# Kernel optimization log

Hardware: AMD Instinct MI355X
Metric: run time of the kernel (lower is better)

The kernel has to match this reference:

```python
import jax, jax.numpy as jnp
import numpy as np

H = 8      # num heads
D = 16     # head dim
HID = 128  # hidden_channels = H*D
L = 2      # num layers
NT = [30000, 15000, 2000]  # compound, protein, herb
# edge types as (src_type_idx, dst_type_idx); node types: 0=compound,1=protein,2=herb
ETYPES = [(2, 0), (0, 2), (0, 1), (1, 0), (1, 1)]


def segment_softmax(a, seg, n):
    m = jax.ops.segment_max(a, seg, num_segments=n)
    e = jnp.exp(a - m[seg])
    s = jax.ops.segment_sum(e, seg, num_segments=n)
    return e / (s[seg] + 1e-16)


def hgt_layer(xs, edges, Wk, bk, Wq, bq, Wv, bv, Wa, ba, skip, a_rel, m_rel, p_rel):
    ns = [x.shape[0] for x in xs]
    k = [(xs[t] @ Wk[t] + bk[t]).reshape(ns[t], H, D) for t in range(3)]
    q = [(xs[t] @ Wq[t] + bq[t]).reshape(ns[t], H, D) for t in range(3)]
    v = [(xs[t] @ Wv[t] + bv[t]).reshape(ns[t], H, D) for t in range(3)]
    out = [jnp.zeros((ns[t], H, D), xs[t].dtype) for t in range(3)]
    scale = 1.0 / np.sqrt(D).astype(np.float32)
    for e, (st, dt) in enumerate(ETYPES):
        src, dst = edges[e]
        # relation-specific key/value transforms per head, then gather per edge
        ke = jnp.einsum('nhd,hde->nhe', k[st], a_rel[e])[src]   # [E,H,D]
        ve = jnp.einsum('nhd,hde->nhe', v[st], m_rel[e])[src]   # [E,H,D]
        qe = q[dt][dst]                                          # [E,H,D]
        alpha = (qe * ke).sum(-1) * p_rel[e] * scale             # [E,H]
        alpha = segment_softmax(alpha, dst, ns[dt])
        out[dt] = out[dt] + jax.ops.segment_sum(alpha[..., None] * ve, dst, num_segments=ns[dt])
    res = []
    for t in range(3):
        o = jax.nn.gelu(out[t].reshape(ns[t], H * D)) @ Wa[t] + ba[t]
        beta = jax.nn.sigmoid(skip[t])
        res.append(beta * o + (1.0 - beta) * xs[t])
    return res


def setup_inputs() -> dict:
    key = jax.random.key(0)
    ks = jax.random.split(key, 40)
    i = 0
    def nk():
        nonlocal i
        i += 1
        return ks[i - 1]
    inp = {}
    inp['x_compound'] = jax.random.normal(nk(), (NT[0], 512), jnp.float32)
    inp['x_protein'] = jax.random.normal(nk(), (NT[1], 1024), jnp.float32)
    inp['x_herb'] = jax.random.normal(nk(), (NT[2], 128), jnp.float32)
    E = [100000, 100000, 200000, 200000, 150000]
    for e, (st, dt) in enumerate(ETYPES):
        inp[f'e{e}_src'] = jax.random.randint(nk(), (E[e],), 0, NT[st], jnp.int32)
        inp[f'e{e}_dst'] = jax.random.randint(nk(), (E[e],), 0, NT[dt], jnp.int32)
    def lin(k, fi, fo):
        return jax.random.normal(k, (fi, fo), jnp.float32) / np.sqrt(fi).astype(np.float32)
    inp['Wc'] = lin(nk(), 512, HID); inp['bc'] = jnp.zeros((HID,), jnp.float32)
    inp['Wp'] = lin(nk(), 1024, HID); inp['bp'] = jnp.zeros((HID,), jnp.float32)
    inp['Wh'] = lin(nk(), 128, HID); inp['bh'] = jnp.zeros((HID,), jnp.float32)
    for nm in ['Wk', 'Wq', 'Wv', 'Wa']:
        inp[nm] = jax.random.normal(nk(), (L, 3, HID, HID), jnp.float32) / np.sqrt(HID).astype(np.float32)
    for nm in ['bk', 'bq', 'bv', 'ba']:
        inp[nm] = jnp.zeros((L, 3, HID), jnp.float32)
    inp['skip'] = jnp.ones((L, 3), jnp.float32)
    inp['a_rel'] = jax.random.normal(nk(), (L, 5, H, D, D), jnp.float32) / np.sqrt(D).astype(np.float32)
    inp['m_rel'] = jax.random.normal(nk(), (L, 5, H, D, D), jnp.float32) / np.sqrt(D).astype(np.float32)
    inp['p_rel'] = jnp.ones((L, 5, H), jnp.float32)
    return inp


def reference(x_compound, x_protein, x_herb,
              e0_src, e0_dst, e1_src, e1_dst, e2_src, e2_dst, e3_src, e3_dst, e4_src, e4_dst,
              Wc, bc, Wp, bp, Wh, bh, Wk, bk, Wq, bq, Wv, bv, Wa, ba, skip, a_rel, m_rel, p_rel):
    xs = [x_compound @ Wc + bc, x_protein @ Wp + bp, x_herb @ Wh + bh]
    edges = [(e0_src, e0_dst), (e1_src, e1_dst), (e2_src, e2_dst), (e3_src, e3_dst), (e4_src, e4_dst)]
    for l in range(L):
        xs = hgt_layer(xs, edges, Wk[l], bk[l], Wq[l], bq[l], Wv[l], bv[l], Wa[l], ba[l],
                       skip[l], a_rel[l], m_rel[l], p_rel[l])
    # concatenate [compound; protein; herb] node embeddings along node axis
    return jnp.concatenate(xs, axis=0)
```

## Files before the change

### kernel.cpp

```cpp
#include <hip/hip_runtime.h>
#include <math.h>

#define HID 128

typedef __bf16 bf16x8 __attribute__((ext_vector_type(8)));
typedef float f32x4 __attribute__((ext_vector_type(4)));

__device__ __forceinline__ float gelu_f(float x) {
    float x3 = x*x*x;
    return 0.5f*x*(1.f + tanhf(0.7978845608028654f*(x + 0.044715f*x3)));
}
__device__ __forceinline__ unsigned short bf16_rn(float x) {
    unsigned int u = __float_as_uint(x);
    unsigned int r = (u + 0x7FFFu + ((u >> 16) & 1u)) >> 16;
    return (unsigned short)r;
}
__device__ __forceinline__ void split2(float x, unsigned short& h, unsigned short& l) {
    h = bf16_rn(x);
    float hf = __uint_as_float(((unsigned int)h) << 16);
    l = bf16_rn(x - hf);
}
__device__ __forceinline__ float blo(unsigned int u){ return __uint_as_float(u << 16); }
__device__ __forceinline__ float bhi(unsigned int u){ return __uint_as_float(u & 0xffff0000u); }

struct WJobs { const float* in[15]; unsigned short* hi[15]; unsigned short* lo[15]; int kbits[15]; };
__global__ __launch_bounds__(256) void wprep(WJobs p) {
    int z = blockIdx.y;
    int kbits = p.kbits[z];
    int K = 1 << kbits;
    int idx = blockIdx.x * 256 + threadIdx.x;
    if (idx >= (K << 7)) return;
    int col = idx >> kbits, k = idx & (K - 1);
    float v = p.in[z][(size_t)k * 128 + col];
    unsigned short h, l; split2(v, h, l);
    p.hi[z][idx] = h; p.lo[z][idx] = l;
}

__global__ __launch_bounds__(256) void fuse_w(const float* __restrict__ Wk, const float* __restrict__ Wv,
        const float* __restrict__ a_rel, const float* __restrict__ m_rel,
        unsigned short* __restrict__ keh, unsigned short* __restrict__ kel,
        unsigned short* __restrict__ veh, unsigned short* __restrict__ vel) {
    const int STm[5] = {2,0,0,1,1};
    int z = blockIdx.y;
    int m = (z < 10) ? z : z - 10;
    const float* W = (z < 10) ? Wk : Wv;
    const float* rel = (z < 10) ? a_rel : m_rel;
    unsigned short* oh = (z < 10) ? keh : veh;
    unsigned short* ol = (z < 10) ? kel : vel;
    int l = m / 5, e = m % 5, st = STm[e];
    int idx = blockIdx.x * 256 + threadIdx.x;
    int col = idx >> 7, c = idx & 127;
    int h = col >> 4, ep = col & 15;
    const float* w = W + (size_t)(l*3 + st) * 16384;
    const float* r = rel + (size_t)m * 2048 + h * 256;
    float s = 0.f;
    #pragma unroll
    for (int d = 0; d < 16; d++) s += w[c * 128 + h * 16 + d] * r[d * 16 + ep];
    unsigned short hh, ll; split2(s, hh, ll);
    oh[(size_t)m * 16384 + idx] = hh;
    ol[(size_t)m * 16384 + idx] = ll;
}

__global__ void fuse_b(const float* __restrict__ bk, const float* __restrict__ bv,
                       const float* __restrict__ a_rel, const float* __restrict__ m_rel,
                       float* __restrict__ obk, float* __restrict__ obv) {
    const int STm[5] = {2,0,0,1,1};
    int z = blockIdx.y;
    int m = (z < 10) ? z : z - 10;
    const float* b = (z < 10) ? bk : bv;
    const float* rel = (z < 10) ? a_rel : m_rel;
    float* ob = (z < 10) ? obk : obv;
    int l = m / 5, e = m % 5, st = STm[e];
    int col = threadIdx.x;
    int h = col >> 4, ep = col & 15;
    const float* bb = b + (l*3 + st) * 128;
    const float* r = rel + (size_t)m * 2048 + h * 256;
    float s = 0.f;
    #pragma unroll
    for (int d = 0; d < 16; d++) s += bb[h*16 + d] * r[d*16 + ep];
    ob[m * 128 + col] = s;
}

struct IJob { const float* A; const unsigned short* Wh; const unsigned short* Wl;
              const float* bias; float* C; int N; int Kfull; int kbeg; int kend; };
struct IJobs { IJob j[4]; };

__global__ __launch_bounds__(256) void gemm_init(IJobs js) {
    IJob jb = js.j[blockIdx.y];
    int brow = blockIdx.x * 64;
    if (brow >= jb.N) return;
    __shared__ unsigned short Ah[2048], Al[2048], Bh[4096], Bl[4096];
    const int tid = threadIdx.x;
    const int wave = tid >> 6, lane = tid & 63;
    const int wr = wave >> 1, wc = wave & 1;
    const int lrow = lane & 15, lkg = lane >> 4;
    const int Kf = jb.Kfull, N = jb.N;

    f32x4 acc[2][4];
    #pragma unroll
    for (int i = 0; i < 2; i++)
        #pragma unroll
        for (int j = 0; j < 4; j++) acc[i][j] = (f32x4){0.f,0.f,0.f,0.f};

    for (int k0 = jb.kbeg; k0 < jb.kend; k0 += 32) {
        #pragma unroll
        for (int it = 0; it < 2; it++) {
            int c = tid + it*256;
            int row = c >> 3, ks = (c & 7) * 4;
            int gr = brow + row; gr = (gr < N) ? gr : (N - 1);
            float4 v = *(const float4*)(jb.A + (size_t)gr * Kf + k0 + ks);
            ushort4 h, l;
            split2(v.x, h.x, l.x); split2(v.y, h.y, l.y);
            split2(v.z, h.z, l.z); split2(v.w, h.w, l.w);
            int o = ((ks >> 3) * 64 + row) * 8 + (ks & 7);
            *(ushort4*)&Ah[o] = h;
            *(ushort4*)&Al[o] = l;
        }
        #pragma unroll
        for (int it = 0; it < 2; it++) {
            int c = tid + it*256;
            int col = c >> 2, ks8 = (c & 3) * 8;
            size_t go = (size_t)col * Kf + k0 + ks8;
            int o = ((ks8 >> 3) * 128 + col) * 8;
            *(uint4*)&Bh[o] = *(const uint4*)(jb.Wh + go);
            *(uint4*)&Bl[o] = *(const uint4*)(jb.Wl + go);
        }
        __syncthreads();
        bf16x8 ah[2], al_[2], bh[4], bl_[4];
        #pragma unroll
        for (int i = 0; i < 2; i++) {
            int o = (lkg*64 + wr*32 + i*16 + lrow) * 8;
            ah[i] = *(const bf16x8*)&Ah[o];
            al_[i] = *(const bf16x8*)&Al[o];
        }
        #pragma unroll
        for (int j = 0; j < 4; j++) {
            int o = (lkg*128 + wc*64 + j*16 + lrow) * 8;
            bh[j] = *(const bf16x8*)&Bh[o];
            bl_[j] = *(const bf16x8*)&Bl[o];
        }
        #pragma unroll
        for (int i = 0; i < 2; i++)
            #pragma unroll
            for (int j = 0; j < 4; j++) {
                acc[i][j] = __builtin_amdgcn_mfma_f32_16x16x32_bf16(ah[i], bh[j], acc[i][j], 0,0,0);
                acc[i][j] = __builtin_amdgcn_mfma_f32_16x16x32_bf16(ah[i], bl_[j], acc[i][j], 0,0,0);
                acc[i][j] = __builtin_amdgcn_mfma_f32_16x16x32_bf16(al_[i], bh[j], acc[i][j], 0,0,0);
            }
        __syncthreads();
    }

    #pragma unroll
    for (int i = 0; i < 2; i++) {
        int rbase = brow + wr*32 + i*16 + (lane >> 4) * 4;
        #pragma unroll
        for (int j = 0; j < 4; j++) {
            int col = wc*64 + j*16 + lrow;
            float bv = jb.bias ? jb.bias[col] : 0.f;
            #pragma unroll
            for (int rr = 0; rr < 4; rr++) {
                int gr = rbase + rr;
                if (gr < N) jb.C[(size_t)gr * 128 + col] = acc[i][j][rr] + bv;
            }
        }
    }
}

struct Job { const unsigned short* Ah; const unsigned short* Al;
             const unsigned short* Wh; const unsigned short* Wl;
             const float* bias; const float* res; const float* skipv;
             void* C; int N; int mode; };
struct Jobs { Job j[13]; };

__global__ __launch_bounds__(256) void gemm_ws(Jobs js) {
    Job jb = js.j[blockIdx.y];
    int brow = blockIdx.x * 64;
    if (brow >= jb.N) return;
    __shared__ unsigned short Ah[2048], Al[2048], Bh[4096], Bl[4096];
    const int tid = threadIdx.x;
    const int wave = tid >> 6, lane = tid & 63;
    const int wr = wave >> 1, wc = wave & 1;
    const int lrow = lane & 15, lkg = lane >> 4;
    const int N = jb.N;

    f32x4 acc[2][4];
    #pragma unroll
    for (int i = 0; i < 2; i++)
        #pragma unroll
        for (int j = 0; j < 4; j++) acc[i][j] = (f32x4){0.f,0.f,0.f,0.f};

    #pragma unroll
    for (int k0 = 0; k0 < 128; k0 += 32) {
        {
            int c = tid;
            int row = c >> 2, ks8 = (c & 3) * 8;
            int gr = brow + row; gr = (gr < N) ? gr : (N - 1);
            size_t ga = (size_t)gr * 128 + k0 + ks8;
            int o = ((ks8 >> 3) * 64 + row) * 8;
            *(uint4*)&Ah[o] = *(const uint4*)(jb.Ah + ga);
            *(uint4*)&Al[o] = *(const uint4*)(jb.Al + ga);
        }
        #pragma unroll
        for (int it = 0; it < 2; it++) {
            int c = tid + it*256;
            int col = c >> 2, ks8 = (c & 3) * 8;
            size_t go = (size_t)col * 128 + k0 + ks8;
            int o = ((ks8 >> 3) * 128 + col) * 8;
            *(uint4*)&Bh[o] = *(const uint4*)(jb.Wh + go);
            *(uint4*)&Bl[o] = *(const uint4*)(jb.Wl + go);
        }
        __syncthreads();
        bf16x8 ah[2], al_[2], bh[4], bl_[4];
        #pragma unroll
        for (int i = 0; i < 2; i++) {
            int o = (lkg*64 + wr*32 + i*16 + lrow) * 8;
            ah[i] = *(const bf16x8*)&Ah[o];
            al_[i] = *(const bf16x8*)&Al[o];
        }
        #pragma unroll
        for (int j = 0; j < 4; j++) {
            int o = (lkg*128 + wc*64 + j*16 + lrow) * 8;
            bh[j] = *(const bf16x8*)&Bh[o];
            bl_[j] = *(const bf16x8*)&Bl[o];
        }
        #pragma unroll
        for (int i = 0; i < 2; i++)
            #pragma unroll
            for (int j = 0; j < 4; j++) {
                acc[i][j] = __builtin_amdgcn_mfma_f32_16x16x32_bf16(ah[i], bh[j], acc[i][j], 0,0,0);
                acc[i][j] = __builtin_amdgcn_mfma_f32_16x16x32_bf16(ah[i], bl_[j], acc[i][j], 0,0,0);
                acc[i][j] = __builtin_amdgcn_mfma_f32_16x16x32_bf16(al_[i], bh[j], acc[i][j], 0,0,0);
            }
        __syncthreads();
    }

    float beta = 0.f;
    if (jb.mode == 1) beta = 1.f / (1.f + __expf(-jb.skipv[0]));
    #pragma unroll
    for (int i = 0; i < 2; i++) {
        int rbase = brow + wr*32 + i*16 + (lane >> 4) * 4;
        #pragma unroll
        for (int j = 0; j < 4; j++) {
            int col = wc*64 + j*16 + lrow;
            float bv = jb.bias[col];
            #pragma unroll
            for (int rr = 0; rr < 4; rr++) {
                int gr = rbase + rr;
                if (gr < N) {
                    float cv = acc[i][j][rr] + bv;
                    if (jb.mode == 2) {
                        ((unsigned short*)jb.C)[(size_t)gr * 128 + col] = bf16_rn(cv);
                    } else {
                        if (jb.mode == 1) {
                            float r = jb.res[(size_t)gr * 128 + col];
                            cv = beta * cv + (1.f - beta) * r;
                        }
                        ((float*)jb.C)[(size_t)gr * 128 + col] = cv;
                    }
                }
            }
        }
    }
}

struct AttnP {
    const unsigned int* q[5];
    const unsigned int* ke[5];
    const unsigned int* ve[5];
    const int* off[5];
    const int* csr[5];
    float* out[5];
    const float* prel;
    int base[6];
    int ndst[5];
};

__global__ __launch_bounds__(256) void attn_fused(AttnP p) {
    int b = blockIdx.x;
    int z = 0;
    #pragma unroll
    for (int k = 1; k < 5; k++) if (b >= p.base[k]) z = k;
    int node = (b - p.base[z]) * 4 + (threadIdx.x >> 6);
    if (node >= p.ndst[z]) return;
    int lane = threadIdx.x & 63;
    int h = lane >> 3;
    int e0 = p.off[z][node], e1 = p.off[z][node + 1];
    if (e0 == e1) return;
    unsigned int qu = p.q[z][(size_t)node * 64 + lane];
    float qx = blo(qu), qy = bhi(qu);
    float pr = p.prel[z * 8 + h] * 0.25f;
    const unsigned int* KE = p.ke[z];
    const unsigned int* VE = p.ve[z];
    const int* srcs = p.csr[z];
    float m = -INFINITY, s = 0.f, ax = 0.f, ay = 0.f;
    int i = e0;
    int sn = srcs[i];
    unsigned int kn = KE[(size_t)sn * 64 + lane];
    unsigned int vn = VE[(size_t)sn * 64 + lane];
    while (true) {
        unsigned int ku = kn, vu = vn;
        ++i;
        if (i < e1) {
            int s2 = srcs[i];
            kn = KE[(size_t)s2 * 64 + lane];
            vn = VE[(size_t)s2 * 64 + lane];
        }
        float part = qx * blo(ku) + qy * bhi(ku);
        part += __shfl_xor(part, 1);
        part += __shfl_xor(part, 2);
        part += __shfl_xor(part, 4);
        float alpha = part * pr;
        float mn = fmaxf(m, alpha);
        float cc = __expf(m - mn);
        float pe = __expf(alpha - mn);
        s = s * cc + pe;
        ax = ax * cc + pe * blo(vu);
        ay = ay * cc + pe * bhi(vu);
        m = mn;
        if (i >= e1) break;
    }
    float inv = 1.f / (s + 1e-16f);
    float* o = p.out[z] + (size_t)node * 128 + lane * 2;
    o[0] = ax * inv;
    o[1] = ay * inv;
}

__global__ __launch_bounds__(256) void presplit_init(const float* __restrict__ pA, const float* __restrict__ pB,
        float* __restrict__ xsA, unsigned short* __restrict__ xh, unsigned short* __restrict__ xl,
        float* __restrict__ oA, float* __restrict__ oB, int n4, int p0, int p1) {
    int i = blockIdx.x * 256 + threadIdx.x;
    if (i >= n4) return;
    float4 v;
    if (i >= p0 && i < p1) {
        float4 a = ((const float4*)pA)[i - p0];
        float4 b = ((const float4*)pB)[i - p0];
        v = make_float4(a.x+b.x, a.y+b.y, a.z+b.z, a.w+b.w);
        ((float4*)xsA)[i] = v;
    } else v = ((const float4*)xsA)[i];
    ushort4 h, l;
    split2(v.x, h.x, l.x); split2(v.y, h.y, l.y);
    split2(v.z, h.z, l.z); split2(v.w, h.w, l.w);
    ((ushort4*)xh)[i] = h; ((ushort4*)xl)[i] = l;
    float4 z4 = make_float4(0.f,0.f,0.f,0.f);
    ((float4*)oA)[i] = z4; ((float4*)oB)[i] = z4;
}

__global__ __launch_bounds__(256) void presplit_plain(const float* __restrict__ x,
        unsigned short* __restrict__ xh, unsigned short* __restrict__ xl,
        float* __restrict__ oA, float* __restrict__ oB, int n4) {
    int i = blockIdx.x * 256 + threadIdx.x;
    if (i >= n4) return;
    float4 v = ((const float4*)x)[i];
    ushort4 h, l;
    split2(v.x, h.x, l.x); split2(v.y, h.y, l.y);
    split2(v.z, h.z, l.z); split2(v.w, h.w, l.w);
    ((ushort4*)xh)[i] = h; ((ushort4*)xl)[i] = l;
    float4 z4 = make_float4(0.f,0.f,0.f,0.f);
    ((float4*)oA)[i] = z4; ((float4*)oB)[i] = z4;
}

__global__ __launch_bounds__(256) void presplit_gelu(const float* __restrict__ oA, const float* __restrict__ oB,
        unsigned short* __restrict__ xh, unsigned short* __restrict__ xl, int n4) {
    int i = blockIdx.x * 256 + threadIdx.x;
    if (i >= n4) return;
    float4 a = ((const float4*)oA)[i];
    float4 b = ((const float4*)oB)[i];
    float4 v = make_float4(gelu_f(a.x+b.x), gelu_f(a.y+b.y), gelu_f(a.z+b.z), gelu_f(a.w+b.w));
    ushort4 h, l;
    split2(v.x, h.x, l.x); split2(v.y, h.y, l.y);
    split2(v.z, h.z, l.z); split2(v.w, h.w, l.w);
    ((ushort4*)xh)[i] = h; ((ushort4*)xl)[i] = l;
}

struct CsrP {
    const int* esrc[5]; const int* edst[5];
    int* cnt[5]; int* off[5]; int* off2[5]; int* csr[5]; int* bsum[5];
    int E[5]; int N[5]; int nb[5];
};

__global__ __launch_bounds__(256) void csr_hist(CsrP p) {
    int z = blockIdx.z;
    int i = blockIdx.x * 256 + threadIdx.x;
    if (i < p.E[z]) atomicAdd(&p.cnt[z][p.edst[z][i]], 1);
}

__global__ __launch_bounds__(256) void csr_p1(CsrP p) {
    int z = blockIdx.z, b = blockIdx.x;
    int N = p.N[z];
    if (b * 1024 >= N) return;
    const int* cnt = p.cnt[z];
    __shared__ int wtot[4];
    int tid = threadIdx.x, lane = tid & 63, w = tid >> 6;
    int base = b * 1024 + tid * 4;
    int s = 0;
    #pragma unroll
    for (int k = 0; k < 4; k++) { int i = base + k; if (i < N) s += cnt[i]; }
    int incl = s;
    #pragma unroll
    for (int o = 1; o < 64; o <<= 1) { int t = __shfl_up(incl, o); if (lane >= o) incl += t; }
    if (lane == 63) wtot[w] = incl;
    __syncthreads();
    if (tid == 0) p.bsum[z][b] = wtot[0] + wtot[1] + wtot[2] + wtot[3];
}

__global__ void csr_p2(CsrP p) {
    int z = blockIdx.z;
    if (threadIdx.x == 0) {
        int nb = p.nb[z]; int run = 0; int* bs = p.bsum[z];
        for (int b = 0; b < nb; b++) { int t = bs[b]; bs[b] = run; run += t; }
        p.off[z][p.N[z]] = run;
        p.off2[z][p.N[z]] = run;
    }
}

__global__ __launch_bounds__(256) void csr_p3(CsrP p) {
    int z = blockIdx.z, b = blockIdx.x;
    int N = p.N[z];
    if (b * 1024 >= N) return;
    const int* cnt = p.cnt[z]; int* off = p.off[z]; int* off2 = p.off2[z];
    __shared__ int wtot[4];
    int tid = threadIdx.x, lane = tid & 63, w = tid >> 6;
    int base = b * 1024 + tid * 4;
    int v0=0,v1=0,v2=0,v3=0;
    if (base+0 < N) v0 = cnt[base+0];
    if (base+1 < N) v1 = cnt[base+1];
    if (base+2 < N) v2 = cnt[base+2];
    if (base+3 < N) v3 = cnt[base+3];
    int tsum = v0+v1+v2+v3;
    int incl = tsum;
    #pragma unroll
    for (int o = 1; o < 64; o <<= 1) { int t = __shfl_up(incl, o); if (lane >= o) incl += t; }
    if (lane == 63) wtot[w] = incl;
    __syncthreads();
    int we = 0;
    for (int k = 0; k < w; k++) we += wtot[k];
    int texcl = we + incl - tsum + p.bsum[z][b];
    int o0 = texcl, o1 = texcl+v0, o2 = texcl+v0+v1, o3 = texcl+v0+v1+v2;
    if (base+0 < N) { off[base+0]=o0; off2[base+0]=o0; }
    if (base+1 < N) { off[base+1]=o1; off2[base+1]=o1; }
    if (base+2 < N) { off[base+2]=o2; off2[base+2]=o2; }
    if (base+3 < N) { off[base+3]=o3; off2[base+3]=o3; }
}

__global__ __launch_bounds__(256) void csr_scatter(CsrP p) {
    int z = blockIdx.z;
    int i = blockIdx.x * 256 + threadIdx.x;
    if (i < p.E[z]) {
        int d = p.edst[z][i];
        int pos = atomicAdd(&p.off2[z][d], 1);
        p.csr[z][pos] = p.esrc[z][i];
    }
}

extern "C" void kernel_launch(void* const* d_in, const int* in_sizes, int n_in,
                              void* d_out, int out_size, void* d_ws, size_t ws_size,
                              hipStream_t stream)
{
    const float* xin[3] = {(const float*)d_in[0], (const float*)d_in[1], (const float*)d_in[2]};
    const int FIN[3] = {512, 1024, 128};
    const int KBITS[3] = {9, 10, 7};
    int ns[3];
    for (int t = 0; t < 3; t++) ns[t] = in_sizes[t] / FIN[t];
    const int* esrc[5]; const int* edst[5]; int E[5];
    for (int e = 0; e < 5; e++) { esrc[e] = (const int*)d_in[3+2*e]; edst[e] = (const int*)d_in[4+2*e]; E[e] = in_sizes[3+2*e]; }
    const float* Win[3] = {(const float*)d_in[13], (const float*)d_in[15], (const float*)d_in[17]};
    const float* bin[3] = {(const float*)d_in[14], (const float*)d_in[16], (const float*)d_in[18]};
    const float* Wk = (const float*)d_in[19]; const float* Wq = (const float*)d_in[20];
    const float* Wv = (const float*)d_in[21]; const float* Wa = (const float*)d_in[22];
    const float* bk = (const float*)d_in[23]; const float* bq = (const float*)d_in[24];
    const float* bv = (const float*)d_in[25]; const float* ba = (const float*)d_in[26];
    const float* skipp = (const float*)d_in[27];
    const float* a_rel = (const float*)d_in[28];
    const float* m_rel = (const float*)d_in[29];
    const float* p_rel = (const float*)d_in[30];

    static const int ST[5] = {2,0,0,1,1}, DT[5] = {0,2,1,0,1};

    int NTOT = ns[0] + ns[1] + ns[2];
    int toff[3] = {0, ns[0], ns[0] + ns[1]};
    int maxN = ns[0]; for (int t = 1; t < 3; t++) if (ns[t] > maxN) maxN = ns[t];
    int maxE = E[0]; for (int e = 1; e < 5; e++) if (E[e] > maxE) maxE = E[e];

    float* fp = (float*)d_ws;
    float* xsA = fp; fp += (size_t)NTOT*HID;
    float* xsB = fp; fp += (size_t)NTOT*HID;
    float* oaccA = fp; fp += (size_t)NTOT*HID;
    float* oaccB = fp; fp += (size_t)NTOT*HID;
    float* pA = fp; fp += (size_t)ns[1]*HID;
    float* pB = fp; fp += (size_t)ns[1]*HID;
    float* bke = fp; fp += 10*128;
    float* bve = fp; fp += 10*128;
    unsigned short* up = (unsigned short*)fp;
    unsigned short* xh = up; up += (size_t)NTOT*HID;
    unsigned short* xl = up; up += (size_t)NTOT*HID;
    unsigned short* qbf = up; up += (size_t)NTOT*HID;
    unsigned short* kebf[5]; unsigned short* vebf[5];
    for (int e = 0; e < 5; e++) {
        kebf[e] = up; up += (size_t)ns[ST[e]]*HID;
        vebf[e] = up; up += (size_t)ns[ST[e]]*HID;
    }
    unsigned short* wih[3]; unsigned short* wil[3];
    for (int t = 0; t < 3; t++) { wih[t] = up; up += (size_t)FIN[t]*HID; wil[t] = up; up += (size_t)FIN[t]*HID; }
    unsigned short* wqh = up; up += 6*16384; unsigned short* wql = up; up += 6*16384;
    unsigned short* wah = up; up += 6*16384; unsigned short* wal = up; up += 6*16384;
    unsigned short* wkeh = up; up += 10*16384; unsigned short* wkel = up; up += 10*16384;
    unsigned short* wveh = up; up += 10*16384; unsigned short* wvel = up; up += 10*16384;
    uintptr_t ip_ = ((uintptr_t)up + 255) & ~(uintptr_t)255;
    int* ip = (int*)ip_;
    int* off[5]; int* off2[5]; int* csrc[5]; int* cntp[5]; int* bsump[5];
    for (int e = 0; e < 5; e++) { off[e] = ip; ip += ns[DT[e]] + 1; }
    for (int e = 0; e < 5; e++) { off2[e] = ip; ip += ns[DT[e]] + 1; }
    for (int e = 0; e < 5; e++) { csrc[e] = ip; ip += E[e]; }
    int* cntbase = ip; int cnt_tot = 0;
    for (int e = 0; e < 5; e++) { cntp[e] = cntbase + cnt_tot; cnt_tot += ns[DT[e]]; }
    ip += cnt_tot;
    for (int e = 0; e < 5; e++) { bsump[e] = ip; ip += 64; }

    WJobs wj;
    for (int t = 0; t < 3; t++) { wj.in[t]=Win[t]; wj.hi[t]=wih[t]; wj.lo[t]=wil[t]; wj.kbits[t]=KBITS[t]; }
    for (int j = 0; j < 6; j++) {
        wj.in[3+j]=Wq + (size_t)j*16384; wj.hi[3+j]=wqh + (size_t)j*16384; wj.lo[3+j]=wql + (size_t)j*16384; wj.kbits[3+j]=7;
        wj.in[9+j]=Wa + (size_t)j*16384; wj.hi[9+j]=wah + (size_t)j*16384; wj.lo[9+j]=wal + (size_t)j*16384; wj.kbits[9+j]=7;
    }
    wprep<<<dim3(512, 15), 256, 0, stream>>>(wj);
    fuse_w<<<dim3(64, 20), 256, 0, stream>>>(Wk, Wv, a_rel, m_rel, wkeh, wkel, wveh, wvel);
    fuse_b<<<dim3(1, 20), 128, 0, stream>>>(bk, bv, a_rel, m_rel, bke, bve);

    CsrP cp;
    for (int e = 0; e < 5; e++) {
        cp.esrc[e]=esrc[e]; cp.edst[e]=edst[e];
        cp.cnt[e]=cntp[e]; cp.off[e]=off[e]; cp.off2[e]=off2[e]; cp.csr[e]=csrc[e]; cp.bsum[e]=bsump[e];
        cp.E[e]=E[e]; cp.N[e]=ns[DT[e]]; cp.nb[e]=(ns[DT[e]] + 1023)/1024;
    }
    int nbmax = (maxN + 1023) / 1024;
    hipMemsetAsync(cntbase, 0, (size_t)cnt_tot * 4, stream);
    csr_hist<<<dim3((maxE+255)/256, 1, 5), 256, 0, stream>>>(cp);
    csr_p1<<<dim3(nbmax, 1, 5), 256, 0, stream>>>(cp);
    csr_p2<<<dim3(1, 1, 5), 64, 0, stream>>>(cp);
    csr_p3<<<dim3(nbmax, 1, 5), 256, 0, stream>>>(cp);
    csr_scatter<<<dim3((maxE+255)/256, 1, 5), 256, 0, stream>>>(cp);

    IJobs ij;
    ij.j[0] = { xin[0], wih[0], wil[0], bin[0], xsA,                         ns[0], 512, 0, 512 };
    ij.j[1] = { xin[2], wih[2], wil[2], bin[2], xsA + (size_t)toff[2]*HID,   ns[2], 128, 0, 128 };
    ij.j[2] = { xin[1], wih[1], wil[1], bin[1], pA,                          ns[1], 1024, 0, 512 };
    ij.j[3] = { xin[1], wih[1], wil[1], nullptr, pB,                         ns[1], 1024, 512, 1024 };
    int gx = (maxN + 63) / 64;
    gemm_init<<<dim3(gx, 4), 256, 0, stream>>>(ij);

    int n4 = NTOT * HID / 4;
    int p0 = toff[1] * (HID/4), p1 = toff[2] * (HID/4);
    int psg = (n4 + 255) / 256;
    presplit_init<<<psg, 256, 0, stream>>>(pA, pB, xsA, xh, xl, oaccA, oaccB, n4, p0, p1);

    float* outp = (float*)d_out;

    int abase[6]; abase[0] = 0;
    for (int e = 0; e < 5; e++) abase[e+1] = abase[e] + (ns[DT[e]] + 3) / 4;
    float* outsel[5] = { oaccA, oaccA + (size_t)toff[2]*HID, oaccA + (size_t)toff[1]*HID,
                         oaccB, oaccB + (size_t)toff[1]*HID };

    for (int l = 0; l < 2; l++) {
        float* cur = (l == 0) ? xsA : xsB;
        if (l == 1) presplit_plain<<<psg, 256, 0, stream>>>(xsB, xh, xl, oaccA, oaccB, n4);

        Jobs js = {};
        int ji = 0;
        for (int t = 0; t < 3; t++) {
            int m = l*3 + t;
            js.j[ji++] = { xh + (size_t)toff[t]*HID, xl + (size_t)toff[t]*HID,
                           wqh + (size_t)m*16384, wql + (size_t)m*16384,
                           bq + (size_t)m*HID, nullptr, nullptr,
                           qbf + (size_t)toff[t]*HID, ns[t], 2 };
            for (int e = 0; e < 5; e++) {
                if (ST[e] != t) continue;
                int mm = l*5 + e;
                js.j[ji++] = { xh + (size_t)toff[t]*HID, xl + (size_t)toff[t]*HID,
                               wkeh + (size_t)mm*16384, wkel + (size_t)mm*16384,
                               bke + mm*128, nullptr, nullptr,
                               kebf[e], ns[t], 2 };
                js.j[ji++] = { xh + (size_t)toff[t]*HID, xl + (size_t)toff[t]*HID,
                               wveh + (size_t)mm*16384, wvel + (size_t)mm*16384,
                               bve + mm*128, nullptr, nullptr,
                               vebf[e], ns[t], 2 };
            }
        }
        gemm_ws<<<dim3(gx, 13), 256, 0, stream>>>(js);

        AttnP ap;
        for (int e = 0; e < 5; e++) {
            ap.q[e] = (const unsigned int*)(qbf + (size_t)toff[DT[e]]*HID);
            ap.ke[e] = (const unsigned int*)kebf[e];
            ap.ve[e] = (const unsigned int*)vebf[e];
            ap.off[e] = off[e]; ap.csr[e] = csrc[e];
            ap.out[e] = outsel[e];
            ap.ndst[e] = ns[DT[e]];
        }
        for (int k = 0; k < 6; k++) ap.base[k] = abase[k];
        ap.prel = p_rel + l*40;
        attn_fused<<<abase[5], 256, 0, stream>>>(ap);

        presplit_gelu<<<psg, 256, 0, stream>>>(oaccA, oaccB, xh, xl, n4);
        Jobs je = {};
        for (int t = 0; t < 3; t++) {
            int m = l*3 + t;
            je.j[t] = { xh + (size_t)toff[t]*HID, xl + (size_t)toff[t]*HID,
                        wah + (size_t)m*16384, wal + (size_t)m*16384,
                        ba + (size_t)m*HID,
                        cur + (size_t)toff[t]*HID, skipp + m,
                        ((l == 0) ? xsB : outp) + (size_t)toff[t]*HID, ns[t], 1 };
        }
        gemm_ws<<<dim3(gx, 3), 256, 0, stream>>>(je);
    }
}
```

Before: 738.1 us.

## Fuse presplit and gelu passes into GEMM prologues and epilogues

Removes the standalone presplit_init, presplit_plain and presplit_gelu kernels. The GEMM epilogues now write the bf16 hi/lo split of their outputs directly, and the output-projection GEMM reads fp32 attention accumulators, sums them, applies gelu and splits them while loading its A tile. The attention kernel now writes zeros for nodes with no edges, so the output buffers no longer need zeroing. It also processes two edges per iteration with two independent online-softmax states that are merged at the end, and gelu uses an exp-based tanh. This cuts kernel launches and full-tensor memory round trips, at the cost of redundant gelu/split work in the GEMM loads (repeated per block) and extra stores in the epilogues.

```diff
diff --git a/kernel.cpp b/kernel.cpp
--- a/kernel.cpp
+++ b/kernel.cpp
@@ -7,8 +7,12 @@
 typedef float f32x4 __attribute__((ext_vector_type(4)));
 
 __device__ __forceinline__ float gelu_f(float x) {
-    float x3 = x*x*x;
-    return 0.5f*x*(1.f + tanhf(0.7978845608028654f*(x + 0.044715f*x3)));
+    float z = 0.7978845608028654f * (x + 0.044715f * x * x * x);
+    float az = fabsf(z);
+    float e = __expf(-2.f * az);
+    float t = (1.f - e) / (1.f + e);
+    t = (z < 0.f) ? -t : t;
+    return 0.5f * x * (1.f + t);
 }
 __device__ __forceinline__ unsigned short bf16_rn(float x) {
     unsigned int u = __float_as_uint(x);
@@ -82,7 +86,8 @@
 }
 
 struct IJob { const float* A; const unsigned short* Wh; const unsigned short* Wl;
-              const float* bias; float* C; int N; int Kfull; int kbeg; int kend; };
+              const float* bias; float* C; unsigned short* Ch; unsigned short* Cl;
+              int N; int Kfull; int kbeg; int kend; };
 struct IJobs { IJob j[4]; };
 
 __global__ __launch_bounds__(256) void gemm_init(IJobs js) {
@@ -160,16 +165,26 @@
             #pragma unroll
             for (int rr = 0; rr < 4; rr++) {
                 int gr = rbase + rr;
-                if (gr < N) jb.C[(size_t)gr * 128 + col] = acc[i][j][rr] + bv;
+                if (gr < N) {
+                    size_t idx = (size_t)gr * 128 + col;
+                    float cv = acc[i][j][rr] + bv;
+                    jb.C[idx] = cv;
+                    if (jb.Ch) {
+                        unsigned short h, l; split2(cv, h, l);
+                        jb.Ch[idx] = h; jb.Cl[idx] = l;
+                    }
+                }
             }
         }
     }
 }
 
 struct Job { const unsigned short* Ah; const unsigned short* Al;
+             const float* A1; const float* A2;
              const unsigned short* Wh; const unsigned short* Wl;
              const float* bias; const float* res; const float* skipv;
-             void* C; int N; int mode; };
+             void* C; unsigned short* Ch; unsigned short* Cl;
+             int N; int mode; };
 struct Jobs { Job j[13]; };
 
 __global__ __launch_bounds__(256) void gemm_ws(Jobs js) {
@@ -191,7 +206,27 @@
 
     #pragma unroll
     for (int k0 = 0; k0 < 128; k0 += 32) {
-        {
+        if (jb.A1) {
+            #pragma unroll
+            for (int it = 0; it < 2; it++) {
+                int c = tid + it*256;
+                int row = c >> 3, ks = (c & 7) * 4;
+                int gr = brow + row; gr = (gr < N) ? gr : (N - 1);
+                size_t ga = (size_t)gr * 128 + k0 + ks;
+                float4 a = *(const float4*)(jb.A1 + ga);
+                if (jb.A2) {
+                    float4 b2 = *(const float4*)(jb.A2 + ga);
+                    a.x += b2.x; a.y += b2.y; a.z += b2.z; a.w += b2.w;
+                }
+                a.x = gelu_f(a.x); a.y = gelu_f(a.y); a.z = gelu_f(a.z); a.w = gelu_f(a.w);
+                ushort4 h, l;
+                split2(a.x, h.x, l.x); split2(a.y, h.y, l.y);
+                split2(a.z, h.z, l.z); split2(a.w, h.w, l.w);
+                int o = ((ks >> 3) * 64 + row) * 8 + (ks & 7);
+                *(ushort4*)&Ah[o] = h;
+                *(ushort4*)&Al[o] = l;
+            }
+        } else {
             int c = tid;
             int row = c >> 2, ks8 = (c & 3) * 8;
             int gr = brow + row; gr = (gr < N) ? gr : (N - 1);
@@ -247,15 +282,20 @@
             for (int rr = 0; rr < 4; rr++) {
                 int gr = rbase + rr;
                 if (gr < N) {
+                    size_t idx = (size_t)gr * 128 + col;
                     float cv = acc[i][j][rr] + bv;
                     if (jb.mode == 2) {
-                        ((unsigned short*)jb.C)[(size_t)gr * 128 + col] = bf16_rn(cv);
+                        ((unsigned short*)jb.C)[idx] = bf16_rn(cv);
                     } else {
                         if (jb.mode == 1) {
-                            float r = jb.res[(size_t)gr * 128 + col];
+                            float r = jb.res[idx];
                             cv = beta * cv + (1.f - beta) * r;
                         }
-                        ((float*)jb.C)[(size_t)gr * 128 + col] = cv;
+                        ((float*)jb.C)[idx] = cv;
+                        if (jb.Ch) {
+                            unsigned short h, l; split2(cv, h, l);
+                            jb.Ch[idx] = h; jb.Cl[idx] = l;
+                        }
                     }
                 }
             }
@@ -283,89 +323,69 @@
     int node = (b - p.base[z]) * 4 + (threadIdx.x >> 6);
     if (node >= p.ndst[z]) return;
     int lane = threadIdx.x & 63;
-    int h = lane >> 3;
     int e0 = p.off[z][node], e1 = p.off[z][node + 1];
-    if (e0 == e1) return;
+    float2* o = (float2*)(p.out[z] + (size_t)node * 128 + lane * 2);
+    if (e0 == e1) { *o = make_float2(0.f, 0.f); return; }
     unsigned int qu = p.q[z][(size_t)node * 64 + lane];
     float qx = blo(qu), qy = bhi(qu);
-    float pr = p.prel[z * 8 + h] * 0.25f;
+    float pr = p.prel[z * 8 + (lane >> 3)] * 0.25f;
     const unsigned int* KE = p.ke[z];
     const unsigned int* VE = p.ve[z];
     const int* srcs = p.csr[z];
-    float m = -INFINITY, s = 0.f, ax = 0.f, ay = 0.f;
+    float m0 = -INFINITY, s0 = 0.f, ax0 = 0.f, ay0 = 0.f;
+    float m1 = -INFINITY, s1 = 0.f, ax1 = 0.f, ay1 = 0.f;
     int i = e0;
-    int sn = srcs[i];
-    unsigned int kn = KE[(size_t)sn * 64 + lane];
-    unsigned int vn = VE[(size_t)sn * 64 + lane];
-    while (true) {
-        unsigned int ku = kn, vu = vn;
-        ++i;
-        if (i < e1) {
-            int s2 = srcs[i];
-            kn = KE[(size_t)s2 * 64 + lane];
-            vn = VE[(size_t)s2 * 64 + lane];
-        }
-        float part = qx * blo(ku) + qy * bhi(ku);
-        part += __shfl_xor(part, 1);
-        part += __shfl_xor(part, 2);
-        part += __shfl_xor(part, 4);
-        float alpha = part * pr;
-        float mn = fmaxf(m, alpha);
-        float cc = __expf(m - mn);
-        float pe = __expf(alpha - mn);
-        s = s * cc + pe;
-        ax = ax * cc + pe * blo(vu);
-        ay = ay * cc + pe * bhi(vu);
-        m = mn;
-        if (i >= e1) break;
-    }
-    float inv = 1.f / (s + 1e-16f);
-    float* o = p.out[z] + (size_t)node * 128 + lane * 2;
-    o[0] = ax * inv;
-    o[1] = ay * inv;
-}
-
-__global__ __launch_bounds__(256) void presplit_init(const float* __restrict__ pA, const float* __restrict__ pB,
-        float* __restrict__ xsA, unsigned short* __restrict__ xh, unsigned short* __restrict__ xl,
-        float* __restrict__ oA, float* __restrict__ oB, int n4, int p0, int p1) {
+    for (; i + 2 <= e1; i += 2) {
+        int sa = srcs[i], sb = srcs[i+1];
+        unsigned int ka = KE[(size_t)sa*64 + lane];
+        unsigned int kb = KE[(size_t)sb*64 + lane];
+        unsigned int va = VE[(size_t)sa*64 + lane];
+        unsigned int vb = VE[(size_t)sb*64 + lane];
+        float pa = qx*blo(ka) + qy*bhi(ka);
+        float pb = qx*blo(kb) + qy*bhi(kb);
+        pa += __shfl_xor(pa, 1); pb += __shfl_xor(pb, 1);
+        pa += __shfl_xor(pa, 2); pb += __shfl_xor(pb, 2);
+        pa += __shfl_xor(pa, 4); pb += __shfl_xor(pb, 4);
+        float aa = pa * pr, ab = pb * pr;
+        if (aa > m0) { float cc = __expf(m0 - aa); s0 *= cc; ax0 *= cc; ay0 *= cc; m0 = aa; }
+        float pea = __expf(aa - m0);
+        s0 += pea; ax0 += pea * blo(va); ay0 += pea * bhi(va);
+        if (ab > m1) { float cc = __expf(m1 - ab); s1 *= cc; ax1 *= cc; ay1 *= cc; m1 = ab; }
+        float peb = __expf(ab - m1);
+        s1 += peb; ax1 += peb * blo(vb); ay1 += peb * bhi(vb);
+    }
+    if (i < e1) {
+        int sa = srcs[i];
+        unsigned int ka = KE[(size_t)sa*64 + lane];
+        unsigned int va = VE[(size_t)sa*64 + lane];
+        float pa = qx*blo(ka) + qy*bhi(ka);
+        pa += __shfl_xor(pa, 1);
+        pa += __shfl_xor(pa, 2);
+        pa += __shfl_xor(pa, 4);
+        float aa = pa * pr;
+        if (aa > m0) { float cc = __expf(m0 - aa); s0 *= cc; ax0 *= cc; ay0 *= cc; m0 = aa; }
+        float pea = __expf(aa - m0);
+        s0 += pea; ax0 += pea * blo(va); ay0 += pea * bhi(va);
+    }
+    if (s1 > 0.f) {
+        float M = fmaxf(m0, m1);
+        float c0 = __expf(m0 - M), c1 = __expf(m1 - M);
+        s0 = s0*c0 + s1*c1;
+        ax0 = ax0*c0 + ax1*c1;
+        ay0 = ay0*c0 + ay1*c1;
+    }
+    float inv = 1.f / (s0 + 1e-16f);
+    *o = make_float2(ax0 * inv, ay0 * inv);
+}
+
+__global__ __launch_bounds__(256) void presplit_prot(const float* __restrict__ pA, const float* __restrict__ pB,
+        float* __restrict__ xs, unsigned short* __restrict__ xh, unsigned short* __restrict__ xl, int n4) {
     int i = blockIdx.x * 256 + threadIdx.x;
     if (i >= n4) return;
-    float4 v;
-    if (i >= p0 && i < p1) {
-        float4 a = ((const float4*)pA)[i - p0];
-        float4 b = ((const float4*)pB)[i - p0];
-        v = make_float4(a.x+b.x, a.y+b.y, a.z+b.z, a.w+b.w);
-        ((float4*)xsA)[i] = v;
-    } else v = ((const float4*)xsA)[i];
-    ushort4 h, l;
-    split2(v.x, h.x, l.x); split2(v.y, h.y, l.y);
-    split2(v.z, h.z, l.z); split2(v.w, h.w, l.w);
-    ((ushort4*)xh)[i] = h; ((ushort4*)xl)[i] = l;
-    float4 z4 = make_float4(0.f,0.f,0.f,0.f);
-    ((float4*)oA)[i] = z4; ((float4*)oB)[i] = z4;
-}
-
-__global__ __launch_bounds__(256) void presplit_plain(const float* __restrict__ x,
-        unsigned short* __restrict__ xh, unsigned short* __restrict__ xl,
-        float* __restrict__ oA, float* __restrict__ oB, int n4) {
-    int i = blockIdx.x * 256 + threadIdx.x;
-    if (i >= n4) return;
-    float4 v = ((const float4*)x)[i];
-    ushort4 h, l;
-    split2(v.x, h.x, l.x); split2(v.y, h.y, l.y);
-    split2(v.z, h.z, l.z); split2(v.w, h.w, l.w);
-    ((ushort4*)xh)[i] = h; ((ushort4*)xl)[i] = l;
-    float4 z4 = make_float4(0.f,0.f,0.f,0.f);
-    ((float4*)oA)[i] = z4; ((float4*)oB)[i] = z4;
-}
-
-__global__ __launch_bounds__(256) void presplit_gelu(const float* __restrict__ oA, const float* __restrict__ oB,
-        unsigned short* __restrict__ xh, unsigned short* __restrict__ xl, int n4) {
-    int i = blockIdx.x * 256 + threadIdx.x;
-    if (i >= n4) return;
-    float4 a = ((const float4*)oA)[i];
-    float4 b = ((const float4*)oB)[i];
-    float4 v = make_float4(gelu_f(a.x+b.x), gelu_f(a.y+b.y), gelu_f(a.z+b.z), gelu_f(a.w+b.w));
+    float4 a = ((const float4*)pA)[i];
+    float4 b = ((const float4*)pB)[i];
+    float4 v = make_float4(a.x+b.x, a.y+b.y, a.z+b.z, a.w+b.w);
+    ((float4*)xs)[i] = v;
     ushort4 h, l;
     split2(v.x, h.x, l.x); split2(v.y, h.y, l.y);
     split2(v.z, h.z, l.z); split2(v.w, h.w, l.w);
@@ -541,17 +561,17 @@
     csr_scatter<<<dim3((maxE+255)/256, 1, 5), 256, 0, stream>>>(cp);
 
     IJobs ij;
-    ij.j[0] = { xin[0], wih[0], wil[0], bin[0], xsA,                         ns[0], 512, 0, 512 };
-    ij.j[1] = { xin[2], wih[2], wil[2], bin[2], xsA + (size_t)toff[2]*HID,   ns[2], 128, 0, 128 };
-    ij.j[2] = { xin[1], wih[1], wil[1], bin[1], pA,                          ns[1], 1024, 0, 512 };
-    ij.j[3] = { xin[1], wih[1], wil[1], nullptr, pB,                         ns[1], 1024, 512, 1024 };
+    ij.j[0] = { xin[0], wih[0], wil[0], bin[0], xsA, xh, xl,                ns[0], 512, 0, 512 };
+    ij.j[1] = { xin[2], wih[2], wil[2], bin[2], xsA + (size_t)toff[2]*HID,
+                xh + (size_t)toff[2]*HID, xl + (size_t)toff[2]*HID,         ns[2], 128, 0, 128 };
+    ij.j[2] = { xin[1], wih[1], wil[1], bin[1], pA, nullptr, nullptr,       ns[1], 1024, 0, 512 };
+    ij.j[3] = { xin[1], wih[1], wil[1], nullptr, pB, nullptr, nullptr,      ns[1], 1024, 512, 1024 };
     int gx = (maxN + 63) / 64;
     gemm_init<<<dim3(gx, 4), 256, 0, stream>>>(ij);
 
-    int n4 = NTOT * HID / 4;
-    int p0 = toff[1] * (HID/4), p1 = toff[2] * (HID/4);
-    int psg = (n4 + 255) / 256;
-    presplit_init<<<psg, 256, 0, stream>>>(pA, pB, xsA, xh, xl, oaccA, oaccB, n4, p0, p1);
+    int pn4 = ns[1] * HID / 4;
+    presplit_prot<<<(pn4+255)/256, 256, 0, stream>>>(pA, pB,
+        xsA + (size_t)toff[1]*HID, xh + (size_t)toff[1]*HID, xl + (size_t)toff[1]*HID, pn4);
 
     float* outp = (float*)d_out;
 
@@ -562,27 +582,26 @@
 
     for (int l = 0; l < 2; l++) {
         float* cur = (l == 0) ? xsA : xsB;
-        if (l == 1) presplit_plain<<<psg, 256, 0, stream>>>(xsB, xh, xl, oaccA, oaccB, n4);
 
         Jobs js = {};
         int ji = 0;
         for (int t = 0; t < 3; t++) {
             int m = l*3 + t;
-            js.j[ji++] = { xh + (size_t)toff[t]*HID, xl + (size_t)toff[t]*HID,
+            js.j[ji++] = { xh + (size_t)toff[t]*HID, xl + (size_t)toff[t]*HID, nullptr, nullptr,
                            wqh + (size_t)m*16384, wql + (size_t)m*16384,
                            bq + (size_t)m*HID, nullptr, nullptr,
-                           qbf + (size_t)toff[t]*HID, ns[t], 2 };
+                           qbf + (size_t)toff[t]*HID, nullptr, nullptr, ns[t], 2 };
             for (int e = 0; e < 5; e++) {
                 if (ST[e] != t) continue;
                 int mm = l*5 + e;
-                js.j[ji++] = { xh + (size_t)toff[t]*HID, xl + (size_t)toff[t]*HID,
+                js.j[ji++] = { xh + (size_t)toff[t]*HID, xl + (size_t)toff[t]*HID, nullptr, nullptr,
                                wkeh + (size_t)mm*16384, wkel + (size_t)mm*16384,
                                bke + mm*128, nullptr, nullptr,
-                               kebf[e], ns[t], 2 };
-                js.j[ji++] = { xh + (size_t)toff[t]*HID, xl + (size_t)toff[t]*HID,
+                               kebf[e], nullptr, nullptr, ns[t], 2 };
+                js.j[ji++] = { xh + (size_t)toff[t]*HID, xl + (size_t)toff[t]*HID, nullptr, nullptr,
                                wveh + (size_t)mm*16384, wvel + (size_t)mm*16384,
                                bve + mm*128, nullptr, nullptr,
-                               vebf[e], ns[t], 2 };
+                               vebf[e], nullptr, nullptr, ns[t], 2 };
             }
         }
         gemm_ws<<<dim3(gx, 13), 256, 0, stream>>>(js);
@@ -600,15 +619,19 @@
         ap.prel = p_rel + l*40;
         attn_fused<<<abase[5], 256, 0, stream>>>(ap);
 
-        presplit_gelu<<<psg, 256, 0, stream>>>(oaccA, oaccB, xh, xl, n4);
         Jobs je = {};
         for (int t = 0; t < 3; t++) {
             int m = l*3 + t;
-            je.j[t] = { xh + (size_t)toff[t]*HID, xl + (size_t)toff[t]*HID,
+            const float* A1 = oaccA + (size_t)toff[t]*HID;
+            const float* A2 = (t == 2) ? nullptr : (oaccB + (size_t)toff[t]*HID);
+            je.j[t] = { nullptr, nullptr, A1, A2,
                         wah + (size_t)m*16384, wal + (size_t)m*16384,
                         ba + (size_t)m*HID,
                         cur + (size_t)toff[t]*HID, skipp + m,
-                        ((l == 0) ? xsB : outp) + (size_t)toff[t]*HID, ns[t], 1 };
+                        ((l == 0) ? xsB : outp) + (size_t)toff[t]*HID,
+                        (l == 0) ? xh + (size_t)toff[t]*HID : nullptr,
+                        (l == 0) ? xl + (size_t)toff[t]*HID : nullptr,
+                        ns[t], 1 };
         }
         gemm_ws<<<dim3(gx, 3), 256, 0, stream>>>(je);
     }
```

Result: faster. 699.4 us (-5.2%).
